# Performance work log

Hardware: AMD Instinct MI355X
Metric: run time of the kernel (lower is better)

## Reference

```python
import jax, jax.numpy as jnp
import numpy as np

EMBEDDING_DIM = 256
WINDOW = 3


def setup_inputs() -> dict:
    key = jax.random.key(0)
    ks = jax.random.split(key, 7)
    B, T, F = 65536, 16, 129
    D = 64  # feature_dim = embedding_dim // 4 = cutoff = int(F*0.5)
    freq_history = jax.random.normal(ks[0], (B, T, F), dtype=jnp.float32)
    # pattern_detector: Linear(D, D) + LayerNorm(D) + GELU
    W1 = jax.random.normal(ks[1], (D, D), dtype=jnp.float32) * (1.0 / np.sqrt(D))
    b1 = jnp.zeros((D,), dtype=jnp.float32)
    gamma = jnp.ones((D,), dtype=jnp.float32)
    beta = jnp.zeros((D,), dtype=jnp.float32)
    # repetition_classifier: Linear(D, 1) + Sigmoid
    W2 = jax.random.normal(ks[2], (D, 1), dtype=jnp.float32) * (1.0 / np.sqrt(D))
    b2 = jnp.zeros((1,), dtype=jnp.float32)
    return {"freq_history": freq_history, "W1": W1, "b1": b1,
            "gamma": gamma, "beta": beta, "W2": W2, "b2": b2}


def reference(freq_history, W1, b1, gamma, beta, W2, b2):
    F = freq_history.shape[2]
    cutoff = int(F * 0.5)  # 64
    # keep last `window_size` steps
    fh = freq_history[:, -WINDOW:, :]  # [B, 3, F]
    # high-frequency magnitude: abs -> clamp -> per-sample standardize -> clamp
    hfm = jnp.clip(jnp.abs(fh[:, :, :cutoff]), 1e-5, 10.0)  # [B, 3, C]
    mean = hfm.mean(axis=(1, 2), keepdims=True)
    std = hfm.std(axis=(1, 2), keepdims=True, ddof=1) + 1e-5  # torch std is unbiased
    hfm = jnp.clip((hfm - mean) / std, -3.0, 3.0)
    # pattern detector on latest frame (dim_adapter is None: input_dim == feature_dim)
    latest = hfm[:, -1, :]  # [B, C]
    h = latest @ W1 + b1
    mu = h.mean(axis=-1, keepdims=True)
    var = h.var(axis=-1, keepdims=True)
    h = (h - mu) * jax.lax.rsqrt(var + 1e-5) * gamma + beta
    h = jax.nn.gelu(h, approximate=False)  # torch default GELU is exact erf
    repetition_scores = jax.nn.sigmoid(h @ W2 + b2)  # [B, 1]
    # DTW similarity: sequences passed have length 1 -> short-circuit branch:
    # dist = ||first - last||_2, similarity = exp(-dist / embedding_dim)
    diff = fh[:, 0, :cutoff] - fh[:, -1, :cutoff]  # [B, C]
    dist = jnp.sqrt(jnp.sum(diff * diff, axis=1))
    dtw_similarity = jnp.exp(-dist / EMBEDDING_DIM)[:, None]  # [B, 1]
    return repetition_scores, dtw_similarity
```

## Files before the change

kernel.cpp:

```cpp
#include <hip/hip_runtime.h>
#include <math.h>

#define TROWS 16
#define FFEAT 129
#define DD    64
#define TILE  64
#define LROW  72

typedef float f32x4 __attribute__((ext_vector_type(4)));
typedef short s16x8 __attribute__((ext_vector_type(8)));
typedef unsigned short u16x4 __attribute__((ext_vector_type(4)));

#define DPP_ADD(x, ctrl)                                                     \
    (x) += __int_as_float(__builtin_amdgcn_update_dpp(                       \
        0, __float_as_int(x), (ctrl), 0xf, 0xf, true))

#define ROW_REDUCE(x)                                                        \
    do {                                                                     \
        DPP_ADD(x, 0x128); DPP_ADD(x, 0x124);                                \
        DPP_ADD(x, 0x122); DPP_ADD(x, 0x121);                                \
    } while (0)

__device__ __forceinline__ unsigned short f32_to_bf16(float f) {
    unsigned int u = __float_as_uint(f);
    return (unsigned short)((u + 0x7fffu + ((u >> 16) & 1u)) >> 16);
}

__device__ __forceinline__ int kperm(int s) {
    return (s >> 2) + ((s & 3) << 4);
}

__device__ __forceinline__ void load12(float v[12], const float* __restrict__ fh,
                                       int b, int ll) {
    const float* base = fh + (size_t)b * (TROWS * FFEAT) + 13 * FFEAT + ll;
    #pragma unroll
    for (int r = 0; r < 3; ++r)
        #pragma unroll
        for (int c = 0; c < 4; ++c)
            v[r * 4 + c] = base[r * FFEAT + 16 * c];
}

__global__ __launch_bounds__(256, 4) void dtw_tracker_kernel(
    const float* __restrict__ fh,
    const float* __restrict__ W1,
    const float* __restrict__ b1,
    const float* __restrict__ gamma,
    const float* __restrict__ beta,
    const float* __restrict__ W2,
    const float* __restrict__ b2,
    float* __restrict__ out,
    int nB)
{
    __shared__ unsigned short sLat[TILE * LROW];

    const int tid  = threadIdx.x;
    const int lane = tid & 63;
    const int wib  = tid >> 6;
    const int n0   = lane & 15;
    const int kg   = lane >> 4;

    s16x8 Bf[2][4];
    #pragma unroll
    for (int h = 0; h < 2; ++h) {
        #pragma unroll
        for (int t = 0; t < 4; ++t) {
            #pragma unroll
            for (int j = 0; j < 8; ++j) {
                const int s = h * 32 + kg * 8 + j;
                const float w = W1[kperm(s) * DD + (n0 + 16 * t)];
                Bf[h][t][j] = (short)f32_to_bf16(w);
            }
        }
    }

    float b1v[4], gv[4], bv[4], w2v[4];
    #pragma unroll
    for (int t = 0; t < 4; ++t) {
        const int nt = n0 + 16 * t;
        b1v[t] = b1[nt]; gv[t] = gamma[nt]; bv[t] = beta[nt]; w2v[t] = W2[nt];
    }
    const float b2s = b2[0];

    const int bbase = blockIdx.x * TILE;
    const int wb    = bbase + wib * 16;
    const int ll    = n0;
    const int g     = kg;

    float cur[12], nxt[12];
    load12(cur, fh, wb + g, ll);

    #pragma unroll
    for (int i = 0; i < 4; ++i) {
        if (i < 3) load12(nxt, fh, wb + 4 * (i + 1) + g, ll);

        float cl[12];
        #pragma unroll
        for (int j = 0; j < 12; ++j)
            cl[j] = fminf(fmaxf(fabsf(cur[j]), 1e-5f), 10.0f);

        float s = 0.0f, sq = 0.0f, dd = 0.0f;
        #pragma unroll
        for (int j = 0; j < 12; ++j) { s += cl[j]; sq = fmaf(cl[j], cl[j], sq); }
        #pragma unroll
        for (int c = 0; c < 4; ++c) {
            const float d = cur[c] - cur[8 + c];
            dd = fmaf(d, d, dd);
        }
        ROW_REDUCE(s); ROW_REDUCE(sq); ROW_REDUCE(dd);

        const float mean = s * (1.0f / 192.0f);
        float var = (sq - s * s * (1.0f / 192.0f)) * (1.0f / 191.0f);
        var = fmaxf(var, 0.0f);
        const float stdv = sqrtf(var) + 1e-5f;
        const float rinv = __fdividef(1.0f, stdv);

        u16x4 pk;
        #pragma unroll
        for (int c = 0; c < 4; ++c) {
            const float lat =
                fminf(fmaxf((cl[8 + c] - mean) * rinv, -3.0f), 3.0f);
            pk[c] = f32_to_bf16(lat);
        }
        const int row = wib * 16 + 4 * i + g;
        *(u16x4*)&sLat[row * LROW + ll * 4] = pk;

        if (ll == 0)
            out[nB + (wb + 4 * i + g)] = __expf(-sqrtf(dd) * (1.0f / 256.0f));

        #pragma unroll
        for (int j = 0; j < 12; ++j) cur[j] = nxt[j];
    }

    const int r = wib * 16 + n0;
    const unsigned short* ar = &sLat[r * LROW + kg * 8];
    const s16x8 a0 = *(const s16x8*)(ar);
    const s16x8 a1 = *(const s16x8*)(ar + 32);

    f32x4 acc[4];
    #pragma unroll
    for (int t = 0; t < 4; ++t) {
        acc[t] = f32x4{0.0f, 0.0f, 0.0f, 0.0f};
        acc[t] = __builtin_amdgcn_mfma_f32_16x16x32_bf16(a0, Bf[0][t], acc[t], 0, 0, 0);
        acc[t] = __builtin_amdgcn_mfma_f32_16x16x32_bf16(a1, Bf[1][t], acc[t], 0, 0, 0);
    }

    #pragma unroll
    for (int q = 0; q < 4; ++q) {
        const float h0 = acc[0][q] + b1v[0];
        const float h1 = acc[1][q] + b1v[1];
        const float h2 = acc[2][q] + b1v[2];
        const float h3 = acc[3][q] + b1v[3];

        float s  = (h0 + h1) + (h2 + h3);
        float ss = fmaf(h0, h0, fmaf(h1, h1, fmaf(h2, h2, h3 * h3)));
        ROW_REDUCE(s); ROW_REDUCE(ss);

        const float mu = s * (1.0f / 64.0f);
        float vv = ss * (1.0f / 64.0f) - mu * mu;
        vv = fmaxf(vv, 0.0f);
        const float rstd = rsqrtf(vv + 1e-5f);

        float sc = 0.0f;
        #pragma unroll
        for (int t = 0; t < 4; ++t) {
            const float hv = (t == 0) ? h0 : (t == 1) ? h1 : (t == 2) ? h2 : h3;
            const float hn = (hv - mu) * rstd * gv[t] + bv[t];
            const float y  = 0.7978845608028654f *
                             fmaf(0.044715f * hn * hn, hn, hn);
            const float ey = __expf(2.0f * y);
            const float th = 1.0f - __fdividef(2.0f, ey + 1.0f);
            const float ge = 0.5f * hn * (1.0f + th);
            sc = fmaf(ge, w2v[t], sc);
        }
        ROW_REDUCE(sc);

        const float rep = __fdividef(1.0f, 1.0f + __expf(-(sc + b2s)));
        if (n0 == q) {
            const int bidx = bbase + wib * 16 + kg * 4 + q;
            out[bidx] = rep;
        }
    }
}

extern "C" void kernel_launch(void* const* d_in, const int* in_sizes, int n_in,
                              void* d_out, int out_size, void* d_ws, size_t ws_size,
                              hipStream_t stream) {
    const float* fh    = (const float*)d_in[0];
    const float* W1    = (const float*)d_in[1];
    const float* b1    = (const float*)d_in[2];
    const float* gamma = (const float*)d_in[3];
    const float* beta  = (const float*)d_in[4];
    const float* W2    = (const float*)d_in[5];
    const float* b2    = (const float*)d_in[6];
    float* out = (float*)d_out;

    const int nB = in_sizes[0] / (TROWS * FFEAT);

    const int nBlocks = nB / TILE;
    dtw_tracker_kernel<<<nBlocks, 256, 0, stream>>>(fh, W1, b1, gamma, beta,
                                                    W2, b2, out, nB);
}
```

Baseline: 25.26 us.

## Split fused kernel into grid-stride stats kernel and separate MLP kernel

Splits the single fused kernel in two. A persistent grid-stride stats kernel computes the per-sample standardization and DTW similarity and writes the bf16 latest-frame vectors to workspace. A second kernel then loads those vectors and runs the MFMA MLP, with the fused kernel kept as a fallback when the workspace is too small. The split is meant to let the memory-bound stats pass run at higher occupancy without the MFMA weight registers. In exchange it adds a second launch and a global round trip of the intermediate activations.

```diff
diff --git a/kernel.cpp b/kernel.cpp
--- a/kernel.cpp
+++ b/kernel.cpp
@@ -40,7 +40,155 @@
             v[r * 4 + c] = base[r * FFEAT + 16 * c];
 }
 
-__global__ __launch_bounds__(256, 4) void dtw_tracker_kernel(
+__device__ __forceinline__ void stats_one(const float v[12], int ll,
+                                          u16x4* pk_out, float* sim_out) {
+    float cl[12];
+    #pragma unroll
+    for (int j = 0; j < 12; ++j)
+        cl[j] = fminf(fmaxf(fabsf(v[j]), 1e-5f), 10.0f);
+
+    float s = 0.0f, sq = 0.0f, dd = 0.0f;
+    #pragma unroll
+    for (int j = 0; j < 12; ++j) { s += cl[j]; sq = fmaf(cl[j], cl[j], sq); }
+    #pragma unroll
+    for (int c = 0; c < 4; ++c) {
+        const float d = v[c] - v[8 + c];
+        dd = fmaf(d, d, dd);
+    }
+    ROW_REDUCE(s); ROW_REDUCE(sq); ROW_REDUCE(dd);
+
+    const float mean = s * (1.0f / 192.0f);
+    float var = (sq - s * s * (1.0f / 192.0f)) * (1.0f / 191.0f);
+    var = fmaxf(var, 0.0f);
+    const float stdv = sqrtf(var) + 1e-5f;
+    const float rinv = __fdividef(1.0f, stdv);
+
+    u16x4 pk;
+    #pragma unroll
+    for (int c = 0; c < 4; ++c) {
+        const float lat = fminf(fmaxf((cl[8 + c] - mean) * rinv, -3.0f), 3.0f);
+        pk[c] = f32_to_bf16(lat);
+    }
+    *pk_out = pk;
+    *sim_out = __expf(-sqrtf(dd) * (1.0f / 256.0f));
+}
+
+__global__ __launch_bounds__(256, 8) void stats_kernel(
+    const float* __restrict__ fh,
+    unsigned short* __restrict__ lat,
+    float* __restrict__ out,
+    int nB)
+{
+    const int tid  = threadIdx.x;
+    const int lane = tid & 63;
+    const int ll   = lane & 15;
+    const int g    = lane >> 4;
+
+    const int wid = (blockIdx.x * 256 + tid) >> 6;
+    const int nW  = (gridDim.x * 256) >> 6;
+    const int nTasks = nB >> 2;
+
+    for (int task = wid; task < nTasks; task += nW) {
+        const int b = task * 4 + g;
+        float v[12];
+        load12(v, fh, b, ll);
+
+        u16x4 pk; float sim;
+        stats_one(v, ll, &pk, &sim);
+
+        *(u16x4*)&lat[(size_t)b * DD + ll * 4] = pk;
+        if (ll == 0) out[nB + b] = sim;
+    }
+}
+
+__global__ __launch_bounds__(256, 4) void mlp_kernel(
+    const unsigned short* __restrict__ lat,
+    const float* __restrict__ W1,
+    const float* __restrict__ b1,
+    const float* __restrict__ gamma,
+    const float* __restrict__ beta,
+    const float* __restrict__ W2,
+    const float* __restrict__ b2,
+    float* __restrict__ out,
+    int nB)
+{
+    const int tid  = threadIdx.x;
+    const int lane = tid & 63;
+    const int wib  = tid >> 6;
+    const int n0   = lane & 15;
+    const int kg   = lane >> 4;
+
+    s16x8 Bf[2][4];
+    #pragma unroll
+    for (int h = 0; h < 2; ++h) {
+        #pragma unroll
+        for (int t = 0; t < 4; ++t) {
+            #pragma unroll
+            for (int j = 0; j < 8; ++j) {
+                const int s = h * 32 + kg * 8 + j;
+                const float w = W1[kperm(s) * DD + (n0 + 16 * t)];
+                Bf[h][t][j] = (short)f32_to_bf16(w);
+            }
+        }
+    }
+    float b1v[4], gv[4], bv[4], w2v[4];
+    #pragma unroll
+    for (int t = 0; t < 4; ++t) {
+        const int nt = n0 + 16 * t;
+        b1v[t] = b1[nt]; gv[t] = gamma[nt]; bv[t] = beta[nt]; w2v[t] = W2[nt];
+    }
+    const float b2s = b2[0];
+
+    const int bbase = blockIdx.x * TILE;
+    const int r = wib * 16 + n0;
+    const unsigned short* ar = lat + (size_t)(bbase + r) * DD + kg * 8;
+    const s16x8 a0 = *(const s16x8*)(ar);
+    const s16x8 a1 = *(const s16x8*)(ar + 32);
+
+    f32x4 acc[4];
+    #pragma unroll
+    for (int t = 0; t < 4; ++t) {
+        acc[t] = f32x4{0.0f, 0.0f, 0.0f, 0.0f};
+        acc[t] = __builtin_amdgcn_mfma_f32_16x16x32_bf16(a0, Bf[0][t], acc[t], 0, 0, 0);
+        acc[t] = __builtin_amdgcn_mfma_f32_16x16x32_bf16(a1, Bf[1][t], acc[t], 0, 0, 0);
+    }
+
+    #pragma unroll
+    for (int q = 0; q < 4; ++q) {
+        const float h0 = acc[0][q] + b1v[0];
+        const float h1 = acc[1][q] + b1v[1];
+        const float h2 = acc[2][q] + b1v[2];
+        const float h3 = acc[3][q] + b1v[3];
+
+        float s  = (h0 + h1) + (h2 + h3);
+        float ss = fmaf(h0, h0, fmaf(h1, h1, fmaf(h2, h2, h3 * h3)));
+        ROW_REDUCE(s); ROW_REDUCE(ss);
+
+        const float mu = s * (1.0f / 64.0f);
+        float vv = ss * (1.0f / 64.0f) - mu * mu;
+        vv = fmaxf(vv, 0.0f);
+        const float rstd = rsqrtf(vv + 1e-5f);
+
+        float sc = 0.0f;
+        #pragma unroll
+        for (int t = 0; t < 4; ++t) {
+            const float hv = (t == 0) ? h0 : (t == 1) ? h1 : (t == 2) ? h2 : h3;
+            const float hn = (hv - mu) * rstd * gv[t] + bv[t];
+            const float y  = 0.7978845608028654f *
+                             fmaf(0.044715f * hn * hn, hn, hn);
+            const float ey = __expf(2.0f * y);
+            const float th = 1.0f - __fdividef(2.0f, ey + 1.0f);
+            const float ge = 0.5f * hn * (1.0f + th);
+            sc = fmaf(ge, w2v[t], sc);
+        }
+        ROW_REDUCE(sc);
+
+        const float rep = __fdividef(1.0f, 1.0f + __expf(-(sc + b2s)));
+        if (n0 == q) out[bbase + wib * 16 + kg * 4 + q] = rep;
+    }
+}
+
+__global__ __launch_bounds__(256, 4) void fused_kernel(
     const float* __restrict__ fh,
     const float* __restrict__ W1,
     const float* __restrict__ b1,
@@ -61,18 +209,14 @@
 
     s16x8 Bf[2][4];
     #pragma unroll
-    for (int h = 0; h < 2; ++h) {
-        #pragma unroll
-        for (int t = 0; t < 4; ++t) {
+    for (int h = 0; h < 2; ++h)
+        #pragma unroll
+        for (int t = 0; t < 4; ++t)
             #pragma unroll
             for (int j = 0; j < 8; ++j) {
                 const int s = h * 32 + kg * 8 + j;
-                const float w = W1[kperm(s) * DD + (n0 + 16 * t)];
-                Bf[h][t][j] = (short)f32_to_bf16(w);
+                Bf[h][t][j] = (short)f32_to_bf16(W1[kperm(s) * DD + (n0 + 16 * t)]);
             }
-        }
-    }
-
     float b1v[4], gv[4], bv[4], w2v[4];
     #pragma unroll
     for (int t = 0; t < 4; ++t) {
@@ -92,41 +236,11 @@
     #pragma unroll
     for (int i = 0; i < 4; ++i) {
         if (i < 3) load12(nxt, fh, wb + 4 * (i + 1) + g, ll);
-
-        float cl[12];
-        #pragma unroll
-        for (int j = 0; j < 12; ++j)
-            cl[j] = fminf(fmaxf(fabsf(cur[j]), 1e-5f), 10.0f);
-
-        float s = 0.0f, sq = 0.0f, dd = 0.0f;
-        #pragma unroll
-        for (int j = 0; j < 12; ++j) { s += cl[j]; sq = fmaf(cl[j], cl[j], sq); }
-        #pragma unroll
-        for (int c = 0; c < 4; ++c) {
-            const float d = cur[c] - cur[8 + c];
-            dd = fmaf(d, d, dd);
-        }
-        ROW_REDUCE(s); ROW_REDUCE(sq); ROW_REDUCE(dd);
-
-        const float mean = s * (1.0f / 192.0f);
-        float var = (sq - s * s * (1.0f / 192.0f)) * (1.0f / 191.0f);
-        var = fmaxf(var, 0.0f);
-        const float stdv = sqrtf(var) + 1e-5f;
-        const float rinv = __fdividef(1.0f, stdv);
-
-        u16x4 pk;
-        #pragma unroll
-        for (int c = 0; c < 4; ++c) {
-            const float lat =
-                fminf(fmaxf((cl[8 + c] - mean) * rinv, -3.0f), 3.0f);
-            pk[c] = f32_to_bf16(lat);
-        }
+        u16x4 pk; float sim;
+        stats_one(cur, ll, &pk, &sim);
         const int row = wib * 16 + 4 * i + g;
         *(u16x4*)&sLat[row * LROW + ll * 4] = pk;
-
-        if (ll == 0)
-            out[nB + (wb + 4 * i + g)] = __expf(-sqrtf(dd) * (1.0f / 256.0f));
-
+        if (ll == 0) out[nB + (wb + 4 * i + g)] = sim;
         #pragma unroll
         for (int j = 0; j < 12; ++j) cur[j] = nxt[j];
     }
@@ -143,42 +257,32 @@
         acc[t] = __builtin_amdgcn_mfma_f32_16x16x32_bf16(a0, Bf[0][t], acc[t], 0, 0, 0);
         acc[t] = __builtin_amdgcn_mfma_f32_16x16x32_bf16(a1, Bf[1][t], acc[t], 0, 0, 0);
     }
-
     #pragma unroll
     for (int q = 0; q < 4; ++q) {
         const float h0 = acc[0][q] + b1v[0];
         const float h1 = acc[1][q] + b1v[1];
         const float h2 = acc[2][q] + b1v[2];
         const float h3 = acc[3][q] + b1v[3];
-
         float s  = (h0 + h1) + (h2 + h3);
         float ss = fmaf(h0, h0, fmaf(h1, h1, fmaf(h2, h2, h3 * h3)));
         ROW_REDUCE(s); ROW_REDUCE(ss);
-
         const float mu = s * (1.0f / 64.0f);
         float vv = ss * (1.0f / 64.0f) - mu * mu;
         vv = fmaxf(vv, 0.0f);
         const float rstd = rsqrtf(vv + 1e-5f);
-
         float sc = 0.0f;
         #pragma unroll
         for (int t = 0; t < 4; ++t) {
             const float hv = (t == 0) ? h0 : (t == 1) ? h1 : (t == 2) ? h2 : h3;
             const float hn = (hv - mu) * rstd * gv[t] + bv[t];
-            const float y  = 0.7978845608028654f *
-                             fmaf(0.044715f * hn * hn, hn, hn);
+            const float y  = 0.7978845608028654f * fmaf(0.044715f * hn * hn, hn, hn);
             const float ey = __expf(2.0f * y);
             const float th = 1.0f - __fdividef(2.0f, ey + 1.0f);
-            const float ge = 0.5f * hn * (1.0f + th);
-            sc = fmaf(ge, w2v[t], sc);
+            sc = fmaf(0.5f * hn * (1.0f + th), w2v[t], sc);
         }
         ROW_REDUCE(sc);
-
         const float rep = __fdividef(1.0f, 1.0f + __expf(-(sc + b2s)));
-        if (n0 == q) {
-            const int bidx = bbase + wib * 16 + kg * 4 + q;
-            out[bidx] = rep;
-        }
+        if (n0 == q) out[bbase + wib * 16 + kg * 4 + q] = rep;
     }
 }
 
@@ -195,8 +299,15 @@
     float* out = (float*)d_out;
 
     const int nB = in_sizes[0] / (TROWS * FFEAT);
-
-    const int nBlocks = nB / TILE;
-    dtw_tracker_kernel<<<nBlocks, 256, 0, stream>>>(fh, W1, b1, gamma, beta,
+    const size_t latBytes = (size_t)nB * DD * sizeof(unsigned short);
+
+    if (ws_size >= latBytes) {
+        unsigned short* lat = (unsigned short*)d_ws;
+        stats_kernel<<<2048, 256, 0, stream>>>(fh, lat, out, nB);
+        mlp_kernel<<<nB / TILE, 256, 0, stream>>>(lat, W1, b1, gamma, beta,
+                                                  W2, b2, out, nB);
+    } else {
+        fused_kernel<<<nB / TILE, 256, 0, stream>>>(fh, W1, b1, gamma, beta,
                                                     W2, b2, out, nB);
-}
+    }
+}
```

Result: slower. 32.83 us (+29.9%).
